# Optimization experiments

Measured on AMD Instinct MI355X. Metric: run time of the kernel, lower is better.

The kernel has to match this reference:

```python
import jax, jax.numpy as jnp
import numpy as np

N = 1_000_000
C = 32
GRID_SIZE = (16, 16, 16, 16, 16)

# Only 4 corners are combined in the original module: dims 0 and 1 vary
# between floor/ceil, dims 2-4 always use floor.
CORNER_OFFSETS = np.array([
    [0, 0, 0, 0, 0],
    [1, 0, 0, 0, 0],
    [0, 1, 0, 0, 0],
    [1, 1, 0, 0, 0],
], dtype=np.int32)  # (4, 5)


def setup_inputs() -> dict:
    key = jax.random.key(0)
    k1, k2 = jax.random.split(key)
    ray = jax.random.uniform(k1, (N, 5), dtype=jnp.float32)
    grid = jax.random.normal(k2, (1, C) + GRID_SIZE, dtype=jnp.float32)
    ray_min = jnp.zeros((5,), dtype=jnp.float32)
    ray_max = jnp.ones((5,), dtype=jnp.float32)
    return {"ray": ray, "grid": grid, "ray_min": ray_min, "ray_max": ray_max}


def reference(ray, grid, ray_min, ray_max):
    dims = np.array(grid.shape[2:], dtype=np.int64)       # (D0..D4)
    C_ = grid.shape[1]
    P = int(np.prod(dims))
    strides = np.array([np.prod(dims[i + 1:]) for i in range(5)], dtype=np.int32)  # (5,)

    # Normalize ray -> fractional grid coordinates, shape (N, 5)
    ind = (ray - ray_min) / (ray_max - ray_min) * (dims.astype(np.float32) - 1.0)
    bottom = jnp.floor(ind).astype(jnp.int32)              # (N, 5)
    w = ind - bottom.astype(ind.dtype)                     # (N, 5) interp weights

    offs = jnp.asarray(CORNER_OFFSETS)                     # (4, 5)
    corner = bottom[None, :, :] + offs[:, None, :]         # (4, N, 5)

    dims_j = jnp.asarray(dims.astype(np.int32))
    valid = jnp.all((corner >= 0) & (corner < dims_j), axis=-1)          # (4, N)
    lin = jnp.sum(corner * jnp.asarray(strides), axis=-1)                # (4, N)
    lin = jnp.clip(lin, 0, P - 1)

    # Per-corner multilinear weights: pick w where offset==1 else (1-w), product over 5 dims
    wsel = jnp.where(offs[:, None, :] == 1, w[None, :, :], 1.0 - w[None, :, :])  # (4, N, 5)
    comb_w = jnp.prod(wsel, axis=-1) * valid.astype(ind.dtype)                   # (4, N)

    grid_flat = grid.reshape(C_, P)                        # (C, P)
    vals = grid_flat[:, lin]                               # (C, 4, N) gather
    out = jnp.einsum('cfn,fn->nc', vals, comb_w)           # (N, C)
    return out
```

## Files before the change

### kernel.cpp

```cpp
#include <hip/hip_runtime.h>
#include <hip/hip_fp16.h>

#define PCELLS (16*16*16*16*16)
#define CCH 32

typedef float f32x4 __attribute__((ext_vector_type(4)));
typedef float f32x4u __attribute__((ext_vector_type(4), aligned(4)));

__device__ __forceinline__ float swz_xor4(float x) {
    return __int_as_float(__builtin_amdgcn_ds_swizzle(__float_as_int(x), 0x101F));
}

__global__ __launch_bounds__(256) void transpose_kernel(
        const float* __restrict__ g, __half* __restrict__ gt) {
    __shared__ float tile[CCH][2][65];
    const int d01b = (blockIdx.x >> 6) * 2;
    const int r0   = (blockIdx.x & 63) * 64;
    const int t    = threadIdx.x;

#pragma unroll
    for (int i = 0; i < 4; ++i) {
        int idx = t + i * 256;
        int c   = idx >> 5;
        int dh  = (idx >> 4) & 1;
        int q   = idx & 15;
        const f32x4 v = __builtin_nontemporal_load(
            (const f32x4*)(g + (size_t)c * PCELLS + (size_t)(d01b + dh) * 4096
                             + r0 + 4 * q));
        *(f32x4*)&tile[c][dh][4 * q] = v;
    }
    __syncthreads();

#pragma unroll
    for (int i = 0; i < 2; ++i) {
        int idx = t + i * 256;
        int r   = idx >> 3;
        int dh  = (idx >> 2) & 1;
        int k   = idx & 3;
        __half2 h[4];
#pragma unroll
        for (int jj = 0; jj < 4; ++jj)
            h[jj] = __floats2half2_rn(tile[8 * k + 2 * jj][dh][r],
                                      tile[8 * k + 2 * jj + 1][dh][r]);
        size_t cell = (size_t)(r0 + r) * 256 + d01b + dh;
        __builtin_nontemporal_store(*(f32x4*)h,
                                    (f32x4*)(gt + cell * CCH + 8 * k));
    }
}

__global__ __launch_bounds__(256) void fused_gather(
        const float* __restrict__ ray, const __half* __restrict__ gt,
        const float* __restrict__ mn, const float* __restrict__ mx,
        float* __restrict__ out, int N) {
    int tid  = blockIdx.x * blockDim.x + threadIdx.x;
    int lane = tid & 63;
    int wv   = tid >> 6;
    int gi   = lane >> 3;
    int j    = lane & 7;
    int n0   = wv * 16 + gi;
    if (n0 >= N) return;
    int  n1   = n0 + 8;
    bool has1 = n1 < N;
    int  n1c  = has1 ? n1 : n0;

    const float* rp0 = ray + (size_t)n0  * 5;
    const float* rp1 = ray + (size_t)n1c * 5;
    float rv0[5], rv1[5];
    *(f32x4u*)rv0 = *(const f32x4u*)rp0;  rv0[4] = rp0[4];
    *(f32x4u*)rv1 = *(const f32x4u*)rp1;  rv1[4] = rp1[4];

    float wa[5], wb[5]; int ba[5], bb[5];
#pragma unroll
    for (int d = 0; d < 5; ++d) {
        float m   = mn[d];
        float inv = __builtin_amdgcn_rcpf(mx[d] - m) * 15.0f;
        float i0  = (rv0[d] - m) * inv;
        float i1  = (rv1[d] - m) * inv;
        float f0 = floorf(i0), f1 = floorf(i1);
        ba[d] = (int)f0;  wa[d] = i0 - f0;
        bb[d] = (int)f1;  wb[d] = i1 - f1;
    }
    float ta = (1.f - wa[2]) * (1.f - wa[3]) * (1.f - wa[4]);
    float tb = (1.f - wb[2]) * (1.f - wb[3]) * (1.f - wb[4]);
    int la = (ba[2] * 256 + ba[3] * 16 + ba[4]) * 256 + ba[0] * 16 + ba[1];
    int lb = (bb[2] * 256 + bb[3] * 16 + bb[4]) * 256 + bb[0] * 16 + bb[1];
    int l0 = min(max(la, 0), PCELLS - 18);
    int l1 = min(max(lb, 0), PCELLS - 18);

    const int h = j >> 2;
    float f10 = h ? wa[1] : 1.f - wa[1];
    float cA0 = (1.f - wa[0]) * ta * f10;
    float cB0 = wa[0] * ta * f10;
    float f11 = h ? wb[1] : 1.f - wb[1];
    float cA1 = (1.f - wb[0]) * tb * f11;
    float cB1 = wb[0] * tb * f11;

    const char* gb = (const char*)gt;
    const size_t off = (size_t)16 * j;
    f32x4 vA0 = *(const f32x4*)(gb + (size_t)l0 * 64 + off);
    f32x4 vB0 = *(const f32x4*)(gb + (size_t)(l0 + 16) * 64 + off);
    f32x4 vA1 = *(const f32x4*)(gb + (size_t)l1 * 64 + off);
    f32x4 vB1 = *(const f32x4*)(gb + (size_t)(l1 + 16) * 64 + off);

    float acc0[8], acc1[8];
    const __half2* hA0 = (const __half2*)&vA0;
    const __half2* hB0 = (const __half2*)&vB0;
    const __half2* hA1 = (const __half2*)&vA1;
    const __half2* hB1 = (const __half2*)&vB1;
#pragma unroll
    for (int k = 0; k < 4; ++k) {
        float2 a0 = __half22float2(hA0[k]);
        float2 b0 = __half22float2(hB0[k]);
        acc0[2 * k]     = cA0 * a0.x + cB0 * b0.x;
        acc0[2 * k + 1] = cA0 * a0.y + cB0 * b0.y;
        float2 a1 = __half22float2(hA1[k]);
        float2 b1 = __half22float2(hB1[k]);
        acc1[2 * k]     = cA1 * a1.x + cB1 * b1.x;
        acc1[2 * k + 1] = cA1 * a1.y + cB1 * b1.y;
    }
#pragma unroll
    for (int k = 0; k < 8; ++k) {
        acc0[k] += swz_xor4(acc0[k]);
        acc1[k] += swz_xor4(acc1[k]);
    }

    const int qo = j & 3;
    f32x4 lo0 = *(f32x4*)&acc0[0], hi0 = *(f32x4*)&acc0[4];
    f32x4 st0 = h ? hi0 : lo0;
    __builtin_nontemporal_store(
        st0, (f32x4*)(out + (size_t)n0 * CCH + 8 * qo + 4 * h));
    if (has1) {
        f32x4 lo1 = *(f32x4*)&acc1[0], hi1 = *(f32x4*)&acc1[4];
        f32x4 st1 = h ? hi1 : lo1;
        __builtin_nontemporal_store(
            st1, (f32x4*)(out + (size_t)n1 * CCH + 8 * qo + 4 * h));
    }
}

__device__ __forceinline__ void ray_corners_orig(
        const float* __restrict__ ray, const float* __restrict__ mn,
        const float* __restrict__ mx, int n, int* lin, float* wt) {
    float w[5]; int b[5];
#pragma unroll
    for (int d = 0; d < 5; ++d) {
        float m   = mn[d];
        float inv = __builtin_amdgcn_rcpf(mx[d] - m) * 15.0f;
        float i0  = (ray[(size_t)n * 5 + d] - m) * inv;
        float f0  = floorf(i0);
        b[d] = (int)f0;  w[d] = i0 - f0;
    }
    float tau = (1.f - w[2]) * (1.f - w[3]) * (1.f - w[4]);
    int rest  = b[2] * 256 + b[3] * 16 + b[4];
    wt[0] = (1.f - w[0]) * (1.f - w[1]) * tau;
    wt[1] = w[0] * (1.f - w[1]) * tau;
    wt[2] = (1.f - w[0]) * w[1] * tau;
    wt[3] = w[0] * w[1] * tau;
    int l00 = b[0] * 65536 + b[1] * 4096 + rest;
    int lv[4] = { l00, l00 + 65536, l00 + 4096, l00 + 65536 + 4096 };
#pragma unroll
    for (int f = 0; f < 4; ++f)
        lin[f] = min(max(lv[f], 0), PCELLS - 1);
}

__global__ __launch_bounds__(256) void direct_kernel(
        const float* __restrict__ ray, const float* __restrict__ g,
        const float* __restrict__ mn, const float* __restrict__ mx,
        float* __restrict__ out, int N) {
    int tid = blockIdx.x * blockDim.x + threadIdx.x;
    int n = tid >> 5;
    int c = tid & 31;
    if (n >= N) return;
    int lin[4]; float wt[4];
    ray_corners_orig(ray, mn, mx, n, lin, wt);
    const float* gc = g + (size_t)c * PCELLS;
    float acc = wt[0] * gc[lin[0]] + wt[1] * gc[lin[1]] +
                wt[2] * gc[lin[2]] + wt[3] * gc[lin[3]];
    out[(size_t)n * CCH + c] = acc;
}

extern "C" void kernel_launch(void* const* d_in, const int* in_sizes, int n_in,
                              void* d_out, int out_size, void* d_ws, size_t ws_size,
                              hipStream_t stream) {
    const float* ray  = (const float*)d_in[0];
    const float* grid = (const float*)d_in[1];
    const float* mn   = (const float*)d_in[2];
    const float* mx   = (const float*)d_in[3];
    float* out = (float*)d_out;
    const int N = in_sizes[0] / 5;

    const size_t gt_bytes = (size_t)PCELLS * CCH * sizeof(__half);

    if (ws_size >= gt_bytes) {
        __half* gt = (__half*)d_ws;
        transpose_kernel<<<PCELLS / 128, 256, 0, stream>>>(grid, gt);

        long long waves   = ((long long)N + 15) / 16;
        long long threads = waves * 64;
        fused_gather<<<(int)((threads + 255) / 256), 256, 0, stream>>>(
            ray, gt, mn, mx, out, N);
    } else {
        long long total = (long long)N * CCH;
        direct_kernel<<<(int)((total + 255) / 256), 256, 0, stream>>>(
            ray, grid, mn, mx, out, N);
    }
}
```

Before: 299.0 us.

## Restructure grid transpose to convert to fp16 before staging in shared memory

Rewrites the grid transpose kernel so each block covers 32 d01 slices by 16 inner cells, converts to fp16 right after the global load, and stages packed halves in padded shared memory. Each thread then writes 16-byte chunks covering contiguous runs of the output layout. The goal is to halve LDS traffic and get larger contiguous stores, so the preprocessing pass costs less. The trade-off is scalar half-word LDS reads with possible bank conflicts and a different block count.

```diff
diff --git a/kernel.cpp b/kernel.cpp
--- a/kernel.cpp
+++ b/kernel.cpp
@@ -11,40 +11,58 @@
     return __int_as_float(__builtin_amdgcn_ds_swizzle(__float_as_int(x), 0x101F));
 }
 
+__device__ __forceinline__ unsigned pack2(float a, float b) {
+    __half2 h = __floats2half2_rn(a, b);
+    return *(unsigned*)&h;
+}
+
 __global__ __launch_bounds__(256) void transpose_kernel(
         const float* __restrict__ g, __half* __restrict__ gt) {
-    __shared__ float tile[CCH][2][65];
-    const int d01b = (blockIdx.x >> 6) * 2;
-    const int r0   = (blockIdx.x & 63) * 64;
-    const int t    = threadIdx.x;
-
-#pragma unroll
-    for (int i = 0; i < 4; ++i) {
-        int idx = t + i * 256;
-        int c   = idx >> 5;
-        int dh  = (idx >> 4) & 1;
-        int q   = idx & 15;
-        const f32x4 v = __builtin_nontemporal_load(
-            (const f32x4*)(g + (size_t)c * PCELLS + (size_t)(d01b + dh) * 4096
-                             + r0 + 4 * q));
-        *(f32x4*)&tile[c][dh][4 * q] = v;
+    __shared__ uint2 hq[32][32][5];
+    const int bx = blockIdx.x;
+    const int db = bx >> 8;
+    const int rt = bx & 255;
+    const int t  = threadIdx.x;
+    const int j  = t & 31;
+
+#pragma unroll
+    for (int rr = 0; rr < 4; ++rr) {
+        int c = (t >> 5) + 8 * rr;
+        const float* src = g + (size_t)c * PCELLS
+                             + (size_t)(db * 32 + j) * 4096 + (size_t)rt * 16;
+        f32x4 v0 = __builtin_nontemporal_load((const f32x4*)(src));
+        f32x4 v1 = __builtin_nontemporal_load((const f32x4*)(src + 4));
+        f32x4 v2 = __builtin_nontemporal_load((const f32x4*)(src + 8));
+        f32x4 v3 = __builtin_nontemporal_load((const f32x4*)(src + 12));
+        uint2 u0, u1, u2, u3;
+        u0.x = pack2(v0[0], v0[1]);  u0.y = pack2(v0[2], v0[3]);
+        u1.x = pack2(v1[0], v1[1]);  u1.y = pack2(v1[2], v1[3]);
+        u2.x = pack2(v2[0], v2[1]);  u2.y = pack2(v2[2], v2[3]);
+        u3.x = pack2(v3[0], v3[1]);  u3.y = pack2(v3[2], v3[3]);
+        hq[c][j][0] = u0;  hq[c][j][1] = u1;
+        hq[c][j][2] = u2;  hq[c][j][3] = u3;
     }
     __syncthreads();
 
-#pragma unroll
-    for (int i = 0; i < 2; ++i) {
-        int idx = t + i * 256;
-        int r   = idx >> 3;
-        int dh  = (idx >> 2) & 1;
-        int k   = idx & 3;
-        __half2 h[4];
-#pragma unroll
-        for (int jj = 0; jj < 4; ++jj)
-            h[jj] = __floats2half2_rn(tile[8 * k + 2 * jj][dh][r],
-                                      tile[8 * k + 2 * jj + 1][dh][r]);
-        size_t cell = (size_t)(r0 + r) * 256 + d01b + dh;
-        __builtin_nontemporal_store(*(f32x4*)h,
-                                    (f32x4*)(gt + cell * CCH + 8 * k));
+    const __half* hl = (const __half*)&hq[0][0][0];
+#pragma unroll
+    for (int m = 0; m < 8; ++m) {
+        int flat = t + 256 * m;
+        int i  = flat >> 7;
+        int u  = flat & 127;
+        int jj = u >> 2;
+        int o  = u & 3;
+        unsigned d[4];
+#pragma unroll
+        for (int dd = 0; dd < 4; ++dd) {
+            __half a = hl[((8 * o + 2 * dd)     * 32 + jj) * 20 + i];
+            __half b = hl[((8 * o + 2 * dd + 1) * 32 + jj) * 20 + i];
+            __half2 hh = __halves2half2(a, b);
+            d[dd] = *(unsigned*)&hh;
+        }
+        size_t byte = (size_t)rt * 262144 + (size_t)db * 2048
+                    + (size_t)i * 16384 + (size_t)u * 16;
+        __builtin_nontemporal_store(*(f32x4*)d, (f32x4*)((char*)gt + byte));
     }
 }
 
@@ -192,7 +210,7 @@
 
     if (ws_size >= gt_bytes) {
         __half* gt = (__half*)d_ws;
-        transpose_kernel<<<PCELLS / 128, 256, 0, stream>>>(grid, gt);
+        transpose_kernel<<<2048, 256, 0, stream>>>(grid, gt);
 
         long long waves   = ((long long)N + 15) / 16;
         long long threads = waves * 64;
```

New measurement: 364.2 us. 21.8% more time.
